# Optimization experiments

Hardware: AMD Instinct MI355X
Metric: run time of the kernel (lower is better)

The kernel has to match this reference:

```python
import math
import jax, jax.numpy as jnp
import numpy as np

D_MODEL = 1024
N_HEAD = 16
D_K = D_MODEL // N_HEAD  # 64
D_V = D_MODEL // N_HEAD  # 64


def setup_inputs() -> dict:
    key = jax.random.key(0)
    kx, kq, kk, kv, ko = jax.random.split(key, 5)
    B, L = 4, 2048
    x = jax.random.normal(kx, (B, L, D_MODEL), dtype=jnp.float32)
    mask = jnp.zeros((B, 1, 1, L), dtype=bool)  # True = masked; all-False here
    s = 1.0 / math.sqrt(D_MODEL)
    # torch nn.Linear weights: shape (out_features, in_features), y = x @ W.T
    Wq = jax.random.normal(kq, (D_K * N_HEAD, D_MODEL), dtype=jnp.float32) * s
    Wk = jax.random.normal(kk, (D_K * N_HEAD, D_MODEL), dtype=jnp.float32) * s
    Wv = jax.random.normal(kv, (D_V * N_HEAD, D_MODEL), dtype=jnp.float32) * s
    Wo = jax.random.normal(ko, (D_MODEL, D_V * N_HEAD), dtype=jnp.float32) * s
    return {"x": x, "mask": mask, "Wq": Wq, "Wk": Wk, "Wv": Wv, "Wo": Wo}


def reference(x, mask, Wq, Wk, Wv, Wo):
    B, L, D = x.shape
    H, Dh, Dv = N_HEAD, D_K, D_V
    # projections (torch Linear: x @ W.T), then split heads -> (B,H,L,Dh)
    q = (x @ Wq.T).reshape(B, L, H, Dh).transpose(0, 2, 1, 3)
    k = (x @ Wk.T).reshape(B, L, H, Dh).transpose(0, 2, 1, 3)
    v = (x @ Wv.T).reshape(B, L, H, Dv).transpose(0, 2, 1, 3)
    scores = jnp.einsum('bhqd,bhkd->bhqk', q, k) / math.sqrt(Dh)
    scores = jnp.where(mask, -jnp.inf, scores)
    attn = jax.nn.softmax(scores, axis=-1)  # dropout p=0.0 -> identity
    out = jnp.einsum('bhqk,bhkd->bhqd', attn, v)  # (B,H,L,Dv)
    out = out.transpose(0, 2, 1, 3).reshape(B, L, H * Dv)
    return out @ Wo.T
```

## Files before the change

kernel.cpp:

```cpp
#include <hip/hip_runtime.h>

typedef __bf16 bf16_t;
typedef __bf16 bf16x4 __attribute__((ext_vector_type(4)));
typedef __bf16 bf16x8 __attribute__((ext_vector_type(8)));
typedef float f32x4 __attribute__((ext_vector_type(4)));

#define MFMA_16x16x32 __builtin_amdgcn_mfma_f32_16x16x32_bf16

#define GLD16(dst_lds, src_glb) \
  __builtin_amdgcn_global_load_lds((__attribute__((address_space(1))) void*)(void*)(src_glb), \
                                   (__attribute__((address_space(3))) void*)(dst_lds), 16, 0, 0)

#define EXP2RAW __builtin_amdgcn_exp2f

#define QSCALE 0.18033688011112042f

__global__ void cvt_all(const float* __restrict__ x,  const float* __restrict__ wq,
                        const float* __restrict__ wk, const float* __restrict__ wv,
                        const float* __restrict__ wo,
                        bf16_t* __restrict__ xb, bf16_t* __restrict__ wqkv,
                        bf16_t* __restrict__ wob) {
    const int XN = 8 * 1024 * 1024, WN = 1024 * 1024;
    int i = (blockIdx.x * blockDim.x + threadIdx.x) * 4;
    const float* s; bf16_t* d; int off;
    if (i < XN)                { s = x;  d = xb;            off = i; }
    else if (i < XN + WN)      { s = wq; d = wqkv;          off = i - XN; }
    else if (i < XN + 2 * WN)  { s = wk; d = wqkv + WN;     off = i - XN - WN; }
    else if (i < XN + 3 * WN)  { s = wv; d = wqkv + 2 * WN; off = i - XN - 2 * WN; }
    else                       { s = wo; d = wob;           off = i - XN - 3 * WN; }
    float4 v = *(const float4*)(s + off);
    bf16x4 o;
    o[0] = (bf16_t)v.x; o[1] = (bf16_t)v.y; o[2] = (bf16_t)v.z; o[3] = (bf16_t)v.w;
    *(bf16x4*)(d + off) = o;
}

__global__ __launch_bounds__(256) void gemm_qkv(
    const bf16_t* __restrict__ A, const bf16_t* __restrict__ W,
    bf16_t* __restrict__ qo, bf16_t* __restrict__ ko, bf16_t* __restrict__ vto)
{
    constexpr int K = 1024, BK = 64;
    __shared__ bf16_t smem[16896];
    bf16_t* As = smem;
    bf16_t* Bs = smem + 8192;
    const int t = threadIdx.x;
    const int lane = t & 63, wave = t >> 6;
    const int quad = lane >> 4, l16 = lane & 15;
    const int m0 = blockIdx.x * 128, n0 = blockIdx.y * 128;
    const int wm = (wave & 1) * 64, wn = (wave >> 1) * 64;

    f32x4 acc[4][4] = {};

    int goff[4];
#pragma unroll
    for (int m = 0; m < 4; ++m) {
        int c = t + m * 256;
        int row = c >> 3;
        goff[m] = row * K + (((c & 7) ^ (row & 7)) * 8);
    }

    for (int k0 = 0; k0 < K; k0 += BK) {
        __syncthreads();
#pragma unroll
        for (int m = 0; m < 4; ++m) {
            int c8 = (t + m * 256) * 8;
            GLD16(As + c8, A + (size_t)m0 * K + k0 + goff[m]);
            GLD16(Bs + c8, W + (size_t)n0 * K + k0 + goff[m]);
        }
        __syncthreads();
#pragma unroll
        for (int half = 0; half < 2; ++half) {
            const int sw = (((half * 4 + quad) ^ (l16 & 7)) * 8);
            bf16x8 af[4], bfr[4];
#pragma unroll
            for (int i = 0; i < 4; ++i)
                af[i] = *(const bf16x8*)(As + (wm + i * 16 + l16) * 64 + sw);
#pragma unroll
            for (int j = 0; j < 4; ++j)
                bfr[j] = *(const bf16x8*)(Bs + (wn + j * 16 + l16) * 64 + sw);
#pragma unroll
            for (int i = 0; i < 4; ++i)
#pragma unroll
                for (int j = 0; j < 4; ++j)
                    acc[i][j] = MFMA_16x16x32(af[i], bfr[j], acc[i][j], 0, 0, 0);
        }
    }

    if (n0 < 2048) {
#pragma unroll
        for (int i = 0; i < 4; ++i) {
#pragma unroll
            for (int j = 0; j < 4; ++j) {
#pragma unroll
                for (int r = 0; r < 4; ++r) {
                    int row = m0 + wm + i * 16 + quad * 4 + r;
                    int col = n0 + wn + j * 16 + l16;
                    float v = acc[i][j][r];
                    int b = row >> 11, l = row & 2047;
                    int sec = col >> 10, c2 = col & 1023;
                    int h = c2 >> 6, dd = c2 & 63;
                    size_t bh = (size_t)b * 16 + h;
                    if (sec == 0) qo[(bh * 2048 + l) * 64 + dd] = (bf16_t)(v * QSCALE);
                    else          ko[(bh * 2048 + l) * 64 + dd] = (bf16_t)v;
                }
            }
        }
    } else {
        __syncthreads();
        const int hh = wave >> 1;
#pragma unroll
        for (int i = 0; i < 4; ++i) {
            int lbase = wm + (i >> 1) * 32;
            int slot0 = quad * 8 + (i & 1) * 4;
#pragma unroll
            for (int j = 0; j < 4; ++j) {
                int dd = j * 16 + l16;
                bf16x4 pk;
#pragma unroll
                for (int r = 0; r < 4; ++r) pk[r] = (bf16_t)acc[i][j][r];
                *(bf16x4*)(smem + (hh * 64 + dd) * 132 + lbase + slot0) = pk;
            }
        }
        __syncthreads();
        const int b = m0 >> 11, lb = m0 & 2047;
        const int h0 = (n0 - 2048) >> 6;
#pragma unroll
        for (int r8 = 0; r8 < 8; ++r8) {
            int c = r8 * 256 + t;
            int ch = c >> 10, cc = c & 1023;
            int dd = cc >> 4, lc = (cc & 15) * 8;
            bf16x8 vv = *(const bf16x8*)(smem + (ch * 64 + dd) * 132 + lc);
            size_t bh = (size_t)b * 16 + h0 + ch;
            *(bf16x8*)(vto + (bh * 64 + dd) * 2048 + lb + lc) = vv;
        }
    }
}

__global__ __launch_bounds__(256) void gemm_out(
    const bf16_t* __restrict__ A, const bf16_t* __restrict__ W,
    float* __restrict__ out)
{
    constexpr int K = 1024, BK = 64;
    __shared__ bf16_t smem[16384];
    bf16_t* As = smem;
    bf16_t* Bs = smem + 8192;
    const int t = threadIdx.x;
    const int lane = t & 63, wave = t >> 6;
    const int quad = lane >> 4, l16 = lane & 15;
    const int m0 = blockIdx.x * 128, n0 = blockIdx.y * 128;
    const int wm = (wave & 1) * 64, wn = (wave >> 1) * 64;

    f32x4 acc[4][4] = {};

    int goff[4];
#pragma unroll
    for (int m = 0; m < 4; ++m) {
        int c = t + m * 256;
        int row = c >> 3;
        goff[m] = row * K + (((c & 7) ^ (row & 7)) * 8);
    }

    for (int k0 = 0; k0 < K; k0 += BK) {
        __syncthreads();
#pragma unroll
        for (int m = 0; m < 4; ++m) {
            int c8 = (t + m * 256) * 8;
            GLD16(As + c8, A + (size_t)m0 * K + k0 + goff[m]);
            GLD16(Bs + c8, W + (size_t)n0 * K + k0 + goff[m]);
        }
        __syncthreads();
#pragma unroll
        for (int half = 0; half < 2; ++half) {
            const int sw = (((half * 4 + quad) ^ (l16 & 7)) * 8);
            bf16x8 af[4], bfr[4];
#pragma unroll
            for (int i = 0; i < 4; ++i)
                af[i] = *(const bf16x8*)(As + (wm + i * 16 + l16) * 64 + sw);
#pragma unroll
            for (int j = 0; j < 4; ++j)
                bfr[j] = *(const bf16x8*)(Bs + (wn + j * 16 + l16) * 64 + sw);
#pragma unroll
            for (int i = 0; i < 4; ++i)
#pragma unroll
                for (int j = 0; j < 4; ++j)
                    acc[i][j] = MFMA_16x16x32(af[i], bfr[j], acc[i][j], 0, 0, 0);
        }
    }

#pragma unroll
    for (int i = 0; i < 4; ++i)
#pragma unroll
        for (int j = 0; j < 4; ++j)
#pragma unroll
            for (int r = 0; r < 4; ++r) {
                int row = m0 + wm + i * 16 + quad * 4 + r;
                int col = n0 + wn + j * 16 + l16;
                out[(size_t)row * 1024 + col] = acc[i][j][r];
            }
}

__global__ __launch_bounds__(256, 2) void attn(
    const bf16_t* __restrict__ q, const bf16_t* __restrict__ k,
    const bf16_t* __restrict__ vt, bf16_t* __restrict__ ho)
{
    constexpr int L = 2048, DH = 64;
    const int bid = blockIdx.x;
    const int bh = bid & 63, qblk = bid >> 6;
    const bf16_t* Q   = q  + (size_t)bh * L * DH;
    const bf16_t* Kg  = k  + (size_t)bh * L * DH;
    const bf16_t* VTg = vt + (size_t)bh * L * DH;
    const int t = threadIdx.x, lane = t & 63, wave = t >> 6;
    const int quad = lane >> 4, l16 = lane & 15;
    const int qrow0 = qblk * 256 + wave * 64;

    __shared__ bf16_t Ks[4][2][2048];
    __shared__ bf16_t Vs[4][2][2048];

    const bf16_t* kga[4];
    const bf16_t* vga[4];
#pragma unroll
    for (int i = 0; i < 4; ++i) {
        int c = i * 64 + lane;
        int slg = (((c & 3) ^ ((c >> 3) & 3)) * 8);
        kga[i] = Kg  + (size_t)((c >> 2) & 31) * DH + (c >> 7) * 32 + slg;
        vga[i] = VTg + (size_t)((c >> 2) & 63) * L + slg;
    }

    bf16x8 bq[4][2];
#pragma unroll
    for (int s4 = 0; s4 < 4; ++s4) {
        bq[s4][0] = *(const bf16x8*)(Q + (size_t)(qrow0 + s4 * 16 + l16) * DH + quad * 8);
        bq[s4][1] = *(const bf16x8*)(Q + (size_t)(qrow0 + s4 * 16 + l16) * DH + 32 + quad * 8);
    }

    bf16x8 vone;
#pragma unroll
    for (int e = 0; e < 8; ++e) vone[e] = (bf16_t)1.0f;

    f32x4 o[4][4] = {};
    f32x4 lsacc[4] = {};

    const int ksw = ((quad ^ ((l16 >> 1) & 3)) * 8);

#pragma unroll
    for (int i = 0; i < 4; ++i) {
        GLD16(&Ks[wave][0][0] + (i * 64 + lane) * 8, kga[i]);
        GLD16(&Vs[wave][0][0] + (i * 64 + lane) * 8, vga[i]);
    }
#pragma unroll
    for (int i = 0; i < 4; ++i) {
        GLD16(&Ks[wave][1][0] + (i * 64 + lane) * 8, kga[i] + 32 * DH);
        GLD16(&Vs[wave][1][0] + (i * 64 + lane) * 8, vga[i] + 32);
    }

    for (int ib = 0; ib < 32; ++ib) {
        const int A = 2 * ib;
        const bf16_t* kbA = &Ks[wave][0][0];
        const bf16_t* vbA = &Vs[wave][0][0];
        const bf16_t* kbB = &Ks[wave][1][0];
        const bf16_t* vbB = &Vs[wave][1][0];

        asm volatile("s_waitcnt vmcnt(8)" ::: "memory");
        bf16x8 akA[2][2], avA[4];
#pragma unroll
        for (int ss = 0; ss < 2; ++ss) {
            akA[ss][0] = *(const bf16x8*)(kbA + (ss * 16 + l16) * 32 + ksw);
            akA[ss][1] = *(const bf16x8*)(kbA + 1024 + (ss * 16 + l16) * 32 + ksw);
        }
#pragma unroll
        for (int tt = 0; tt < 4; ++tt)
            avA[tt] = *(const bf16x8*)(vbA + (tt * 16 + l16) * 32 + ksw);

        f32x4 stA[4][2];
        __builtin_amdgcn_s_setprio(1);
#pragma unroll
        for (int q4 = 0; q4 < 4; ++q4)
#pragma unroll
            for (int ss = 0; ss < 2; ++ss) {
                f32x4 z = {};
                z = MFMA_16x16x32(akA[ss][0], bq[q4][0], z, 0, 0, 0);
                stA[q4][ss] = MFMA_16x16x32(akA[ss][1], bq[q4][1], z, 0, 0, 0);
            }
        __builtin_amdgcn_s_setprio(0);

        if (ib < 31) {
            asm volatile("s_waitcnt lgkmcnt(0)" ::: "memory");
            const size_t koff = (size_t)(A + 2) * 32 * DH;
            const int voff = (A + 2) * 32;
#pragma unroll
            for (int i = 0; i < 4; ++i) {
                GLD16(&Ks[wave][0][0] + (i * 64 + lane) * 8, kga[i] + koff);
                GLD16(&Vs[wave][0][0] + (i * 64 + lane) * 8, vga[i] + voff);
            }
            asm volatile("s_waitcnt vmcnt(8)" ::: "memory");
        } else {
            asm volatile("s_waitcnt vmcnt(0)" ::: "memory");
        }

        bf16x8 akB[2][2], avB[4];
#pragma unroll
        for (int ss = 0; ss < 2; ++ss) {
            akB[ss][0] = *(const bf16x8*)(kbB + (ss * 16 + l16) * 32 + ksw);
            akB[ss][1] = *(const bf16x8*)(kbB + 1024 + (ss * 16 + l16) * 32 + ksw);
        }
#pragma unroll
        for (int tt = 0; tt < 4; ++tt)
            avB[tt] = *(const bf16x8*)(vbB + (tt * 16 + l16) * 32 + ksw);

        bf16x8 pA[4];
#pragma unroll
        for (int q4 = 0; q4 < 4; ++q4)
#pragma unroll
            for (int r = 0; r < 4; ++r) {
                float e0 = EXP2RAW(stA[q4][0][r]);
                float e1 = EXP2RAW(stA[q4][1][r]);
                pA[q4][r]     = (bf16_t)e0;
                pA[q4][4 + r] = (bf16_t)e1;
            }

        f32x4 stB[4][2];
        __builtin_amdgcn_s_setprio(1);
#pragma unroll
        for (int q4 = 0; q4 < 4; ++q4)
#pragma unroll
            for (int ss = 0; ss < 2; ++ss) {
                f32x4 z = {};
                z = MFMA_16x16x32(akB[ss][0], bq[q4][0], z, 0, 0, 0);
                stB[q4][ss] = MFMA_16x16x32(akB[ss][1], bq[q4][1], z, 0, 0, 0);
            }
        __builtin_amdgcn_s_setprio(0);

        if (ib < 31) {
            asm volatile("s_waitcnt lgkmcnt(0)" ::: "memory");
            const size_t koff = (size_t)(A + 3) * 32 * DH;
            const int voff = (A + 3) * 32;
#pragma unroll
            for (int i = 0; i < 4; ++i) {
                GLD16(&Ks[wave][1][0] + (i * 64 + lane) * 8, kga[i] + koff);
                GLD16(&Vs[wave][1][0] + (i * 64 + lane) * 8, vga[i] + voff);
            }
        }

        __builtin_amdgcn_s_setprio(1);
#pragma unroll
        for (int q4 = 0; q4 < 4; ++q4)
            lsacc[q4] = MFMA_16x16x32(vone, pA[q4], lsacc[q4], 0, 0, 0);
#pragma unroll
        for (int tt = 0; tt < 4; ++tt)
#pragma unroll
            for (int q4 = 0; q4 < 4; ++q4)
                o[q4][tt] = MFMA_16x16x32(avA[tt], pA[q4], o[q4][tt], 0, 0, 0);
        __builtin_amdgcn_s_setprio(0);

        bf16x8 pB[4];
#pragma unroll
        for (int q4 = 0; q4 < 4; ++q4)
#pragma unroll
            for (int r = 0; r < 4; ++r) {
                float e0 = EXP2RAW(stB[q4][0][r]);
                float e1 = EXP2RAW(stB[q4][1][r]);
                pB[q4][r]     = (bf16_t)e0;
                pB[q4][4 + r] = (bf16_t)e1;
            }

        __builtin_amdgcn_s_setprio(1);
#pragma unroll
        for (int q4 = 0; q4 < 4; ++q4)
            lsacc[q4] = MFMA_16x16x32(vone, pB[q4], lsacc[q4], 0, 0, 0);
#pragma unroll
        for (int tt = 0; tt < 4; ++tt)
#pragma unroll
            for (int q4 = 0; q4 < 4; ++q4)
                o[q4][tt] = MFMA_16x16x32(avB[tt], pB[q4], o[q4][tt], 0, 0, 0);
        __builtin_amdgcn_s_setprio(0);
    }

    const int b = bh >> 4, hd = bh & 15;
#pragma unroll
    for (int q4 = 0; q4 < 4; ++q4) {
        const float inv = 1.0f / lsacc[q4][0];
        const int tok = b * 2048 + qrow0 + q4 * 16 + l16;
#pragma unroll
        for (int tt = 0; tt < 4; ++tt) {
            bf16x4 ov;
#pragma unroll
            for (int r = 0; r < 4; ++r) ov[r] = (bf16_t)(o[q4][tt][r] * inv);
            *(bf16x4*)(ho + (size_t)tok * 1024 + hd * 64 + tt * 16 + quad * 4) = ov;
        }
    }
}

extern "C" void kernel_launch(void* const* d_in, const int* in_sizes, int n_in,
                              void* d_out, int out_size, void* d_ws, size_t ws_size,
                              hipStream_t stream) {
    const float* x  = (const float*)d_in[0];
    const float* Wq = (const float*)d_in[2];
    const float* Wk = (const float*)d_in[3];
    const float* Wv = (const float*)d_in[4];
    const float* Wo = (const float*)d_in[5];
    float* out = (float*)d_out;

    bf16_t* ws   = (bf16_t*)d_ws;
    bf16_t* xb   = ws;
    bf16_t* wqkv = xb   + (size_t)8192 * 1024;
    bf16_t* wob  = wqkv + (size_t)3072 * 1024;
    bf16_t* qb   = wob  + (size_t)1024 * 1024;
    bf16_t* kb   = qb   + (size_t)8192 * 1024;
    bf16_t* vtb  = kb   + (size_t)8192 * 1024;
    bf16_t* hob  = vtb  + (size_t)8192 * 1024;

    cvt_all<<<12288, 256, 0, stream>>>(x, Wq, Wk, Wv, Wo, xb, wqkv, wob);
    gemm_qkv<<<dim3(64, 24), 256, 0, stream>>>(xb, wqkv, qb, kb, vtb);
    attn<<<512, 256, 0, stream>>>(qb, kb, vtb, hob);
    gemm_out<<<dim3(64, 8), 256, 0, stream>>>(hob, wob, out);
}
```

Measured before the change: 252.4 us.

## Software-pipeline attention loop so QK of next tile overlaps exp and PV of previous

Restructures the flash-attention inner loop into a prologue, a steady-state loop and an epilogue. Each iteration computes the exp of the previous tile's scores while loading the next K/V from LDS, then issues the next QK MFMAs together with the previous tile's PV MFMAs. sched_group_barrier hints interleave the exp/VALU work with LDS reads and MFMAs, so the transcendental work hides under matrix-core time. It keeps more score and V registers live at once, which risks register pressure and reduced occupancy, and the buffer refetch clamps the index at the last tile.

```diff
diff --git a/kernel.cpp b/kernel.cpp
--- a/kernel.cpp
+++ b/kernel.cpp
@@ -252,126 +252,178 @@
         GLD16(&Vs[wave][1][0] + (i * 64 + lane) * 8, vga[i] + 32);
     }
 
-    for (int ib = 0; ib < 32; ++ib) {
-        const int A = 2 * ib;
-        const bf16_t* kbA = &Ks[wave][0][0];
-        const bf16_t* vbA = &Vs[wave][0][0];
-        const bf16_t* kbB = &Ks[wave][1][0];
-        const bf16_t* vbB = &Vs[wave][1][0];
-
+    f32x4 stP[4][2];
+    bf16x8 avP[4];
+
+    {
         asm volatile("s_waitcnt vmcnt(8)" ::: "memory");
-        bf16x8 akA[2][2], avA[4];
+        const bf16_t* kb = &Ks[wave][0][0];
+        const bf16_t* vb = &Vs[wave][0][0];
+        bf16x8 ak[2][2];
 #pragma unroll
         for (int ss = 0; ss < 2; ++ss) {
-            akA[ss][0] = *(const bf16x8*)(kbA + (ss * 16 + l16) * 32 + ksw);
-            akA[ss][1] = *(const bf16x8*)(kbA + 1024 + (ss * 16 + l16) * 32 + ksw);
-        }
-#pragma unroll
-        for (int tt = 0; tt < 4; ++tt)
-            avA[tt] = *(const bf16x8*)(vbA + (tt * 16 + l16) * 32 + ksw);
-
-        f32x4 stA[4][2];
-        __builtin_amdgcn_s_setprio(1);
+            ak[ss][0] = *(const bf16x8*)(kb + (ss * 16 + l16) * 32 + ksw);
+            ak[ss][1] = *(const bf16x8*)(kb + 1024 + (ss * 16 + l16) * 32 + ksw);
+        }
+#pragma unroll
+        for (int tt = 0; tt < 4; ++tt)
+            avP[tt] = *(const bf16x8*)(vb + (tt * 16 + l16) * 32 + ksw);
+        asm volatile("s_waitcnt lgkmcnt(0)" ::: "memory");
+#pragma unroll
+        for (int i = 0; i < 4; ++i) {
+            GLD16(&Ks[wave][0][0] + (i * 64 + lane) * 8, kga[i] + (size_t)2 * 32 * DH);
+            GLD16(&Vs[wave][0][0] + (i * 64 + lane) * 8, vga[i] + 2 * 32);
+        }
 #pragma unroll
         for (int q4 = 0; q4 < 4; ++q4)
 #pragma unroll
             for (int ss = 0; ss < 2; ++ss) {
                 f32x4 z = {};
-                z = MFMA_16x16x32(akA[ss][0], bq[q4][0], z, 0, 0, 0);
-                stA[q4][ss] = MFMA_16x16x32(akA[ss][1], bq[q4][1], z, 0, 0, 0);
-            }
-        __builtin_amdgcn_s_setprio(0);
-
-        if (ib < 31) {
-            asm volatile("s_waitcnt lgkmcnt(0)" ::: "memory");
-            const size_t koff = (size_t)(A + 2) * 32 * DH;
-            const int voff = (A + 2) * 32;
-#pragma unroll
-            for (int i = 0; i < 4; ++i) {
-                GLD16(&Ks[wave][0][0] + (i * 64 + lane) * 8, kga[i] + koff);
-                GLD16(&Vs[wave][0][0] + (i * 64 + lane) * 8, vga[i] + voff);
-            }
-            asm volatile("s_waitcnt vmcnt(8)" ::: "memory");
-        } else {
-            asm volatile("s_waitcnt vmcnt(0)" ::: "memory");
-        }
-
-        bf16x8 akB[2][2], avB[4];
+                z = MFMA_16x16x32(ak[ss][0], bq[q4][0], z, 0, 0, 0);
+                stP[q4][ss] = MFMA_16x16x32(ak[ss][1], bq[q4][1], z, 0, 0, 0);
+            }
+    }
+
+    for (int i = 1; i < 63; ++i) {
+        const bf16_t* kb = &Ks[wave][i & 1][0];
+        const bf16_t* vb = &Vs[wave][i & 1][0];
+        asm volatile("s_waitcnt vmcnt(8)" ::: "memory");
+
+        bf16x8 pP[4];
+#pragma unroll
+        for (int q4 = 0; q4 < 4; ++q4)
+#pragma unroll
+            for (int r = 0; r < 4; ++r) {
+                float e0 = EXP2RAW(stP[q4][0][r]);
+                float e1 = EXP2RAW(stP[q4][1][r]);
+                pP[q4][r]     = (bf16_t)e0;
+                pP[q4][4 + r] = (bf16_t)e1;
+            }
+        bf16x8 ak[2][2], avN[4];
 #pragma unroll
         for (int ss = 0; ss < 2; ++ss) {
-            akB[ss][0] = *(const bf16x8*)(kbB + (ss * 16 + l16) * 32 + ksw);
-            akB[ss][1] = *(const bf16x8*)(kbB + 1024 + (ss * 16 + l16) * 32 + ksw);
-        }
-#pragma unroll
-        for (int tt = 0; tt < 4; ++tt)
-            avB[tt] = *(const bf16x8*)(vbB + (tt * 16 + l16) * 32 + ksw);
-
-        bf16x8 pA[4];
-#pragma unroll
-        for (int q4 = 0; q4 < 4; ++q4)
-#pragma unroll
-            for (int r = 0; r < 4; ++r) {
-                float e0 = EXP2RAW(stA[q4][0][r]);
-                float e1 = EXP2RAW(stA[q4][1][r]);
-                pA[q4][r]     = (bf16_t)e0;
-                pA[q4][4 + r] = (bf16_t)e1;
-            }
-
-        f32x4 stB[4][2];
+            ak[ss][0] = *(const bf16x8*)(kb + (ss * 16 + l16) * 32 + ksw);
+            ak[ss][1] = *(const bf16x8*)(kb + 1024 + (ss * 16 + l16) * 32 + ksw);
+        }
+#pragma unroll
+        for (int tt = 0; tt < 4; ++tt)
+            avN[tt] = *(const bf16x8*)(vb + (tt * 16 + l16) * 32 + ksw);
+#pragma unroll
+        for (int g = 0; g < 8; ++g) {
+            __builtin_amdgcn_sched_group_barrier(0x100, 1, 0);
+            __builtin_amdgcn_sched_group_barrier(0x002, 3, 0);
+        }
+
+        asm volatile("s_waitcnt lgkmcnt(0)" ::: "memory");
+        {
+            int nc = i + 2; if (nc > 63) nc = 63;
+            const size_t koff = (size_t)nc * 32 * DH;
+            const int voff = nc * 32;
+#pragma unroll
+            for (int ii = 0; ii < 4; ++ii) {
+                GLD16(&Ks[wave][i & 1][0] + (ii * 64 + lane) * 8, kga[ii] + koff);
+                GLD16(&Vs[wave][i & 1][0] + (ii * 64 + lane) * 8, vga[ii] + voff);
+            }
+        }
+
+        f32x4 stN[4][2];
         __builtin_amdgcn_s_setprio(1);
 #pragma unroll
         for (int q4 = 0; q4 < 4; ++q4)
 #pragma unroll
             for (int ss = 0; ss < 2; ++ss) {
                 f32x4 z = {};
-                z = MFMA_16x16x32(akB[ss][0], bq[q4][0], z, 0, 0, 0);
-                stB[q4][ss] = MFMA_16x16x32(akB[ss][1], bq[q4][1], z, 0, 0, 0);
-            }
+                z = MFMA_16x16x32(ak[ss][0], bq[q4][0], z, 0, 0, 0);
+                stN[q4][ss] = MFMA_16x16x32(ak[ss][1], bq[q4][1], z, 0, 0, 0);
+            }
+#pragma unroll
+        for (int q4 = 0; q4 < 4; ++q4)
+            lsacc[q4] = MFMA_16x16x32(vone, pP[q4], lsacc[q4], 0, 0, 0);
+#pragma unroll
+        for (int tt = 0; tt < 4; ++tt)
+#pragma unroll
+            for (int q4 = 0; q4 < 4; ++q4)
+                o[q4][tt] = MFMA_16x16x32(avP[tt], pP[q4], o[q4][tt], 0, 0, 0);
         __builtin_amdgcn_s_setprio(0);
-
-        if (ib < 31) {
-            asm volatile("s_waitcnt lgkmcnt(0)" ::: "memory");
-            const size_t koff = (size_t)(A + 3) * 32 * DH;
-            const int voff = (A + 3) * 32;
-#pragma unroll
-            for (int i = 0; i < 4; ++i) {
-                GLD16(&Ks[wave][1][0] + (i * 64 + lane) * 8, kga[i] + koff);
-                GLD16(&Vs[wave][1][0] + (i * 64 + lane) * 8, vga[i] + voff);
-            }
-        }
-
+#pragma unroll
+        for (int g = 0; g < 36; ++g) {
+            __builtin_amdgcn_sched_group_barrier(0x008, 1, 0);
+            __builtin_amdgcn_sched_group_barrier(0x002, 1, 0);
+        }
+
+#pragma unroll
+        for (int q4 = 0; q4 < 4; ++q4) { stP[q4][0] = stN[q4][0]; stP[q4][1] = stN[q4][1]; }
+#pragma unroll
+        for (int tt = 0; tt < 4; ++tt) avP[tt] = avN[tt];
+    }
+
+    {
+        const bf16_t* kb = &Ks[wave][1][0];
+        const bf16_t* vb = &Vs[wave][1][0];
+        asm volatile("s_waitcnt vmcnt(0)" ::: "memory");
+        bf16x8 pP[4];
+#pragma unroll
+        for (int q4 = 0; q4 < 4; ++q4)
+#pragma unroll
+            for (int r = 0; r < 4; ++r) {
+                float e0 = EXP2RAW(stP[q4][0][r]);
+                float e1 = EXP2RAW(stP[q4][1][r]);
+                pP[q4][r]     = (bf16_t)e0;
+                pP[q4][4 + r] = (bf16_t)e1;
+            }
+        bf16x8 ak[2][2], avN[4];
+#pragma unroll
+        for (int ss = 0; ss < 2; ++ss) {
+            ak[ss][0] = *(const bf16x8*)(kb + (ss * 16 + l16) * 32 + ksw);
+            ak[ss][1] = *(const bf16x8*)(kb + 1024 + (ss * 16 + l16) * 32 + ksw);
+        }
+#pragma unroll
+        for (int tt = 0; tt < 4; ++tt)
+            avN[tt] = *(const bf16x8*)(vb + (tt * 16 + l16) * 32 + ksw);
+        f32x4 stN[4][2];
         __builtin_amdgcn_s_setprio(1);
 #pragma unroll
         for (int q4 = 0; q4 < 4; ++q4)
-            lsacc[q4] = MFMA_16x16x32(vone, pA[q4], lsacc[q4], 0, 0, 0);
+#pragma unroll
+            for (int ss = 0; ss < 2; ++ss) {
+                f32x4 z = {};
+                z = MFMA_16x16x32(ak[ss][0], bq[q4][0], z, 0, 0, 0);
+                stN[q4][ss] = MFMA_16x16x32(ak[ss][1], bq[q4][1], z, 0, 0, 0);
+            }
+#pragma unroll
+        for (int q4 = 0; q4 < 4; ++q4)
+            lsacc[q4] = MFMA_16x16x32(vone, pP[q4], lsacc[q4], 0, 0, 0);
 #pragma unroll
         for (int tt = 0; tt < 4; ++tt)
 #pragma unroll
             for (int q4 = 0; q4 < 4; ++q4)
-                o[q4][tt] = MFMA_16x16x32(avA[tt], pA[q4], o[q4][tt], 0, 0, 0);
+                o[q4][tt] = MFMA_16x16x32(avP[tt], pP[q4], o[q4][tt], 0, 0, 0);
         __builtin_amdgcn_s_setprio(0);
-
-        bf16x8 pB[4];
+#pragma unroll
+        for (int q4 = 0; q4 < 4; ++q4) { stP[q4][0] = stN[q4][0]; stP[q4][1] = stN[q4][1]; }
+#pragma unroll
+        for (int tt = 0; tt < 4; ++tt) avP[tt] = avN[tt];
+    }
+
+    {
+        bf16x8 pP[4];
 #pragma unroll
         for (int q4 = 0; q4 < 4; ++q4)
 #pragma unroll
             for (int r = 0; r < 4; ++r) {
-                float e0 = EXP2RAW(stB[q4][0][r]);
-                float e1 = EXP2RAW(stB[q4][1][r]);
-                pB[q4][r]     = (bf16_t)e0;
-                pB[q4][4 + r] = (bf16_t)e1;
-            }
-
-        __builtin_amdgcn_s_setprio(1);
-#pragma unroll
-        for (int q4 = 0; q4 < 4; ++q4)
-            lsacc[q4] = MFMA_16x16x32(vone, pB[q4], lsacc[q4], 0, 0, 0);
+                float e0 = EXP2RAW(stP[q4][0][r]);
+                float e1 = EXP2RAW(stP[q4][1][r]);
+                pP[q4][r]     = (bf16_t)e0;
+                pP[q4][4 + r] = (bf16_t)e1;
+            }
+#pragma unroll
+        for (int q4 = 0; q4 < 4; ++q4)
+            lsacc[q4] = MFMA_16x16x32(vone, pP[q4], lsacc[q4], 0, 0, 0);
 #pragma unroll
         for (int tt = 0; tt < 4; ++tt)
 #pragma unroll
             for (int q4 = 0; q4 < 4; ++q4)
-                o[q4][tt] = MFMA_16x16x32(avB[tt], pB[q4], o[q4][tt], 0, 0, 0);
-        __builtin_amdgcn_s_setprio(0);
+                o[q4][tt] = MFMA_16x16x32(avP[tt], pP[q4], o[q4][tt], 0, 0, 0);
     }
 
     const int b = bh >> 4, hd = bh & 15;
```

After: 249.5 us. Within noise of the previous version (-1.2%).
